# Performance work log

Hardware: AMD Instinct MI355X
Metric: run time of the kernel (lower is better)

The kernel has to match this reference:

```python
import jax, jax.numpy as jnp
import numpy as np

KERNEL = (8, 8)
STRIDE = (4, 4)


def setup_inputs() -> dict:
    key = jax.random.key(0)
    x = jax.random.normal(key, (8, 32, 8, 8, 4096), dtype=jnp.float32)
    return {"x": x}


def reference(x):
    b, c, k1, k2, l = x.shape
    s1, s2 = STRIDE
    n = round(l ** 0.5)  # patch grid is n x n (row-major: i outer, j inner)
    h = s1 * (n - 1) + k1
    w = s2 * (n - 1) + k2
    # b c k1 k2 (n n) -> indexable per kernel offset
    xp = x.reshape(b, c, k1, k2, n, n)
    out = jnp.zeros((b, c, h, w), dtype=x.dtype)
    # For a fixed kernel offset (di, dj), the target positions p*s+di are a
    # non-overlapping strided slice, so each add is a disjoint scatter.
    for di in range(k1):
        for dj in range(k2):
            out = out.at[:, :, di:di + s1 * n:s1, dj:dj + s2 * n:s2].add(
                xp[:, :, di, dj])
    return out
```

## Files before the change

kernel.cpp:

```cpp
#include <hip/hip_runtime.h>


#define L      4096
#define NP     64
#define H_OUT  260

typedef float vfloat4 __attribute__((ext_vector_type(4)));

__global__ __launch_bounds__(256) void fold_kernel(const float* __restrict__ x,
                                                   float* __restrict__ out) {
    __shared__ float lds[8192];

    int bid = blockIdx.x;
    int H   = bid & 7;
    int r   = (bid >> 3) & 3;
    int bc  = bid >> 5;

    int lane = threadIdx.x & 63;
    int wv   = threadIdx.x >> 6;

    #pragma unroll
    for (int ci = 0; ci < 4; ++ci) {
        int c   = 4 * wv + ci;
        int isB = c >> 3;
        int p   = c & 7;
        int di  = r + 4 * isB;
        long gb = ((long)(bc * 64 + di * 8 + p)) * L + (long)(8 * H - isB) * 64;
        const float* gp = x + gb + lane * 4;
        float* lp = lds + c * 512;
        #pragma unroll
        for (int k = 0; k < 2; ++k) {
            __builtin_amdgcn_global_load_lds(
                (const __attribute__((address_space(1))) void*)(gp + k * 256),
                (__attribute__((address_space(3))) void*)(lp + k * 256),
                16, 0, 0);
        }
    }
    __syncthreads();

    int t   = threadIdx.x;
    int ii  = t >> 5;
    int ug  = t & 31;
    int ip  = 8 * H + ii;
    bool bvalid = (ip >= 1);
    bool odd    = (ug & 1);
    int  f      = ug >> 1;

    const vfloat4* l4 = (const vfloat4*)lds;
    const vfloat4 vz = {0.f, 0.f, 0.f, 0.f};

    vfloat4 o0, o1, tl;
    #pragma unroll
    for (int s = 0; s < 4; ++s) {
        int ai  = s * 128 + ii * 16 + f;
        int bi  = 1024 + ai;
        int ahi = (s + 4) * 128 + ii * 16 + f;
        int bhi = 1024 + ahi;

        vfloat4 alo = l4[ai];
        vfloat4 blo = bvalid ? l4[bi] : vz;
        vfloat4 ahc = l4[ahi];
        vfloat4 bhc = bvalid ? l4[bhi] : vz;
        float ap3 = (!odd && ug > 0) ? l4[ahi - 1][3] : 0.f;
        float bp3 = (!odd && ug > 0 && bvalid) ? l4[bhi - 1][3] : 0.f;

        float lo0 = odd ? (alo[2] + blo[2]) : (alo[0] + blo[0]);
        float hi0 = odd ? (ahc[1] + bhc[1]) : (ap3 + bp3);
        float lo1 = odd ? (alo[3] + blo[3]) : (alo[1] + blo[1]);
        float hi1 = odd ? (ahc[2] + bhc[2]) : (ahc[0] + bhc[0]);

        o0[s] = lo0 + hi0;
        o1[s] = lo1 + hi1;
        tl[s] = ahc[3] + bhc[3];
    }

    long orow = ((long)(bc * H_OUT) + (4 * ip + r)) * H_OUT;
    vfloat4* op = (vfloat4*)(out + orow);
    op[2 * ug + 0] = o0;
    op[2 * ug + 1] = o1;
    if (ug == 31) {
        op[64] = tl;
    }

    if (H == 7 && t < 65) {
        int u = t;
        const float* pb = x + ((long)(bc * 64 + (r + 4) * 8)) * L + 63 * 64;
        vfloat4 v;
        #pragma unroll
        for (int s = 0; s < 4; ++s) {
            float lo = (u <= 63) ? pb[(long)s * L + u] : 0.f;
            float hi = (u >= 1) ? pb[(long)(s + 4) * L + u - 1] : 0.f;
            v[s] = lo + hi;
        }
        ((vfloat4*)(out + ((long)(bc * H_OUT) + 256 + r) * H_OUT))[u] = v;
    }
}

extern "C" void kernel_launch(void* const* d_in, const int* in_sizes, int n_in,
                              void* d_out, int out_size, void* d_ws, size_t ws_size,
                              hipStream_t stream) {
    const float* x = (const float*)d_in[0];
    float* out     = (float*)d_out;

    fold_kernel<<<8192, 256, 0, stream>>>(x, out);
}
```

Baseline: 363.1 us.

## Loop each block over eight row tiles with double-buffered async LDS loads

The grid shrinks from 8192 to 1024 blocks. Each block now walks the eight H tiles for its (bc, r) pair and prefetches the next tile into a second LDS buffer with global_load_lds while it computes and stores the current one. The goal is to overlap global loads with compute and stores and to cut per-block launch overhead. In exchange, LDS use per block doubles to 64 KB, fewer blocks are resident, and the explicit vmcnt waits may also stall on earlier stores.

```diff
diff --git a/kernel.cpp b/kernel.cpp
--- a/kernel.cpp
+++ b/kernel.cpp
@@ -2,87 +2,99 @@
 
 
 #define L      4096
-#define NP     64
 #define H_OUT  260
 
 typedef float vfloat4 __attribute__((ext_vector_type(4)));
 
 __global__ __launch_bounds__(256) void fold_kernel(const float* __restrict__ x,
                                                    float* __restrict__ out) {
-    __shared__ float lds[8192];
+    __shared__ float lds[16384];
 
     int bid = blockIdx.x;
-    int H   = bid & 7;
-    int r   = (bid >> 3) & 3;
-    int bc  = bid >> 5;
+    int bc  = bid & 255;
+    int r   = bid >> 8;
 
-    int lane = threadIdx.x & 63;
-    int wv   = threadIdx.x >> 6;
+    int t    = threadIdx.x;
+    int lane = t & 63;
+    int wv   = t >> 6;
 
-    #pragma unroll
-    for (int ci = 0; ci < 4; ++ci) {
-        int c   = 4 * wv + ci;
-        int isB = c >> 3;
-        int p   = c & 7;
-        int di  = r + 4 * isB;
-        long gb = ((long)(bc * 64 + di * 8 + p)) * L + (long)(8 * H - isB) * 64;
-        const float* gp = x + gb + lane * 4;
-        float* lp = lds + c * 512;
+    auto stage = [&](int T, int buf) {
         #pragma unroll
-        for (int k = 0; k < 2; ++k) {
-            __builtin_amdgcn_global_load_lds(
-                (const __attribute__((address_space(1))) void*)(gp + k * 256),
-                (__attribute__((address_space(3))) void*)(lp + k * 256),
-                16, 0, 0);
+        for (int ci = 0; ci < 4; ++ci) {
+            int c   = 4 * wv + ci;
+            int isB = c >> 3;
+            int p   = c & 7;
+            int di  = r + 4 * isB;
+            long gb = ((long)(bc * 64 + di * 8 + p)) * L + (long)(8 * T - isB) * 64;
+            const float* gp = x + gb + lane * 4;
+            float* lp = lds + buf * 8192 + c * 512;
+            #pragma unroll
+            for (int k = 0; k < 2; ++k) {
+                __builtin_amdgcn_global_load_lds(
+                    (const __attribute__((address_space(1))) void*)(gp + k * 256),
+                    (__attribute__((address_space(3))) void*)(lp + k * 256),
+                    16, 0, 0);
+            }
         }
-    }
-    __syncthreads();
+    };
 
-    int t   = threadIdx.x;
-    int ii  = t >> 5;
-    int ug  = t & 31;
-    int ip  = 8 * H + ii;
-    bool bvalid = (ip >= 1);
-    bool odd    = (ug & 1);
-    int  f      = ug >> 1;
+    stage(0, 0);
 
-    const vfloat4* l4 = (const vfloat4*)lds;
+    int ii   = t >> 5;
+    int ug   = t & 31;
+    bool odd = (ug & 1);
+    int  f   = ug >> 1;
+
     const vfloat4 vz = {0.f, 0.f, 0.f, 0.f};
 
-    vfloat4 o0, o1, tl;
-    #pragma unroll
-    for (int s = 0; s < 4; ++s) {
-        int ai  = s * 128 + ii * 16 + f;
-        int bi  = 1024 + ai;
-        int ahi = (s + 4) * 128 + ii * 16 + f;
-        int bhi = 1024 + ahi;
+    for (int T = 0; T < 8; ++T) {
+        if (T < 7) {
+            stage(T + 1, (T + 1) & 1);
+            asm volatile("s_waitcnt vmcnt(8)" ::: "memory");
+        } else {
+            asm volatile("s_waitcnt vmcnt(0)" ::: "memory");
+        }
+        __builtin_amdgcn_s_barrier();
 
-        vfloat4 alo = l4[ai];
-        vfloat4 blo = bvalid ? l4[bi] : vz;
-        vfloat4 ahc = l4[ahi];
-        vfloat4 bhc = bvalid ? l4[bhi] : vz;
-        float ap3 = (!odd && ug > 0) ? l4[ahi - 1][3] : 0.f;
-        float bp3 = (!odd && ug > 0 && bvalid) ? l4[bhi - 1][3] : 0.f;
+        const vfloat4* l4 = (const vfloat4*)(lds + (T & 1) * 8192);
+        int ip = 8 * T + ii;
+        bool bvalid = (ip >= 1);
 
-        float lo0 = odd ? (alo[2] + blo[2]) : (alo[0] + blo[0]);
-        float hi0 = odd ? (ahc[1] + bhc[1]) : (ap3 + bp3);
-        float lo1 = odd ? (alo[3] + blo[3]) : (alo[1] + blo[1]);
-        float hi1 = odd ? (ahc[2] + bhc[2]) : (ahc[0] + bhc[0]);
+        vfloat4 o0, o1, tl;
+        #pragma unroll
+        for (int s = 0; s < 4; ++s) {
+            int ai  = s * 128 + ii * 16 + f;
+            int bi  = 1024 + ai;
+            int ahi = (s + 4) * 128 + ii * 16 + f;
+            int bhi = 1024 + ahi;
 
-        o0[s] = lo0 + hi0;
-        o1[s] = lo1 + hi1;
-        tl[s] = ahc[3] + bhc[3];
+            vfloat4 alo = l4[ai];
+            vfloat4 blo = bvalid ? l4[bi] : vz;
+            vfloat4 ahc = l4[ahi];
+            vfloat4 bhc = bvalid ? l4[bhi] : vz;
+            float ap3 = (!odd && ug > 0) ? l4[ahi - 1][3] : 0.f;
+            float bp3 = (!odd && ug > 0 && bvalid) ? l4[bhi - 1][3] : 0.f;
+
+            float lo0 = odd ? (alo[2] + blo[2]) : (alo[0] + blo[0]);
+            float hi0 = odd ? (ahc[1] + bhc[1]) : (ap3 + bp3);
+            float lo1 = odd ? (alo[3] + blo[3]) : (alo[1] + blo[1]);
+            float hi1 = odd ? (ahc[2] + bhc[2]) : (ahc[0] + bhc[0]);
+
+            o0[s] = lo0 + hi0;
+            o1[s] = lo1 + hi1;
+            tl[s] = ahc[3] + bhc[3];
+        }
+
+        long orow = ((long)(bc * H_OUT) + (4 * ip + r)) * H_OUT;
+        vfloat4* op = (vfloat4*)(out + orow);
+        op[2 * ug + 0] = o0;
+        op[2 * ug + 1] = o1;
+        if (ug == 31) op[64] = tl;
+
+        __builtin_amdgcn_s_barrier();
     }
 
-    long orow = ((long)(bc * H_OUT) + (4 * ip + r)) * H_OUT;
-    vfloat4* op = (vfloat4*)(out + orow);
-    op[2 * ug + 0] = o0;
-    op[2 * ug + 1] = o1;
-    if (ug == 31) {
-        op[64] = tl;
-    }
-
-    if (H == 7 && t < 65) {
+    if (t < 65) {
         int u = t;
         const float* pb = x + ((long)(bc * 64 + (r + 4) * 8)) * L + 63 * 64;
         vfloat4 v;
@@ -102,5 +114,5 @@
     const float* x = (const float*)d_in[0];
     float* out     = (float*)d_out;
 
-    fold_kernel<<<8192, 256, 0, stream>>>(x, out);
+    fold_kernel<<<1024, 256, 0, stream>>>(x, out);
 }
```

Result: slower. 380.3 us (+4.7%).
